# Kernel tuning notes

Measured on AMD Instinct MI355X. Metric: run time of the kernel, lower is better.

The kernel has to match this reference:

```python
import jax, jax.numpy as jnp
import numpy as np

K_MASK = -2.3819763e+38
B, T, D = 2, 2048, 2048
N, K, H = 8, 2, 256          # query heads, kv heads, head dim
F = 8192                     # ffn hidden
A = 4                        # num_altup_inputs
P = 4                        # num_modalities
WINDOW = 512
SOFT_CAP = 50.0
Q_SCALE = H ** -0.5
ROPE_BASE = 10000.0


def rms_norm(x, scale=None, eps=1e-6):
    y = x * jax.lax.rsqrt(jnp.mean(jnp.square(x), axis=-1, keepdims=True) + eps)
    if scale is not None:
        y = y * (1.0 + scale)   # scale_plus_one=True
    return y


def apply_rope(x, pos, base=ROPE_BASE, scale_factor=1.0):
    # x: [B,T,num_heads,H], pos: [B,T]
    h = x.shape[-1]
    frac = 2.0 * jnp.arange(h // 2, dtype=jnp.float32) / h
    timescale = base ** frac
    sin_inp = (pos[..., None].astype(jnp.float32) / timescale)[..., None, :] / scale_factor  # [B,T,1,H/2]
    sin, cos = jnp.sin(sin_inp), jnp.cos(sin_inp)
    x1, x2 = jnp.split(x, 2, axis=-1)
    return jnp.concatenate([x1 * cos - x2 * sin, x2 * cos + x1 * sin], axis=-1).astype(x.dtype)


def setup_inputs():
    key = jax.random.key(0)
    ks = jax.random.split(key, 12)
    r = lambda i, shape, s=0.02: jax.random.normal(ks[i], shape, dtype=jnp.float32) * s
    pos = jnp.broadcast_to(jnp.arange(T, dtype=jnp.int32), (B, T))
    causal = pos[:, :, None] >= pos[:, None, :]  # [B,T,T] bool
    return dict(
        x=jax.random.normal(ks[0], (A, B, T, D), dtype=jnp.float32),
        segment_pos=pos,
        attn_mask=causal,
        router_w=r(1, (D, P), 1.0),
        pred_coefs=r(2, (P, A, A), 0.0001),
        corr_coefs=r(3, (P, A), 0.01),
        correct_output_scale=jnp.ones((D,), jnp.float32),
        pre_attn_scale=jnp.zeros((D,), jnp.float32),
        q_w=r(4, (N, D, H)),
        kv_w=r(5, (2, K, D, H)),
        qk_q_scale=jnp.zeros((H,), jnp.float32),
        qk_k_scale=jnp.zeros((H,), jnp.float32),
        o_w=r(6, (N, H, D)),
        post_attn_scale=jnp.zeros((D,), jnp.float32),
        pre_ffw_scale=jnp.zeros((D,), jnp.float32),
        gate_w=r(7, (D, F)),
        up_w=r(8, (D, F)),
        down_w=r(9, (F, D)),
        post_ffw_scale=jnp.zeros((D,), jnp.float32),
    )


def _router(h, router_w):
    # modality router: scale by 1/d_model, project, tanh in fp32
    return jnp.tanh(jnp.einsum('btd,dp->btp', h * (1.0 / D), router_w).astype(jnp.float32))


def _attention(x, segment_pos, attn_mask, q_w, kv_w, qk_q_scale, qk_k_scale, o_w):
    q = jnp.einsum('btd,ndh->btnh', x, q_w)               # [B,T,N,H]
    k, v = jnp.einsum('bsd,ckdh->cbskh', x, kv_w)         # each [B,T,K,H]
    q = rms_norm(q, qk_q_scale)                           # qk norm
    k = rms_norm(k, qk_k_scale)
    v = rms_norm(v)                                       # value norm (no scale)
    q = apply_rope(q, segment_pos) * Q_SCALE
    k = apply_rope(k, segment_pos)
    g = N // K                                            # GQA group size
    qr = q.reshape(B, T, K, g, H)
    logits = jnp.einsum('btkgh,bskh->btkgs', qr, k).reshape(B, T, N, T)
    logits = jnp.tanh(logits / SOFT_CAP) * SOFT_CAP       # attn_logits_soft_cap
    # sliding-window mask combined with causal attn_mask
    sliding = (segment_pos[:, None, :] > segment_pos[:, :, None] - WINDOW) & \
              (segment_pos[:, None, :] < segment_pos[:, :, None] + WINDOW)
    mask = attn_mask & sliding
    padded = jnp.where(mask[:, :, None, :], logits, K_MASK)
    probs = jax.nn.softmax(padded, axis=-1).astype(k.dtype)
    enc = jnp.einsum('btkgs,bskh->btkgh', probs.reshape(B, T, K, g, T), v).reshape(B, T, N, H)
    return jnp.einsum('btnh,nhd->btd', enc, o_w)


def reference(x, segment_pos, attn_mask, router_w, pred_coefs, corr_coefs,
              correct_output_scale, pre_attn_scale, q_w, kv_w, qk_q_scale, qk_k_scale,
              o_w, post_attn_scale, pre_ffw_scale, gate_w, up_w, down_w, post_ffw_scale):
    # ---- AltUp predict ----
    mods = _router(x[0], router_w)                                   # [B,T,P]
    coefs = jnp.einsum('btp,pij->btij', mods, pred_coefs.astype(jnp.float32))
    predictions = x + jnp.einsum('btij,jbtd->ibtd', coefs, x).astype(x.dtype)
    active = predictions[0]
    # ---- attention block ----
    attn_in = rms_norm(active, pre_attn_scale)
    attn = _attention(attn_in, segment_pos, attn_mask, q_w, kv_w, qk_q_scale, qk_k_scale, o_w)
    attn = rms_norm(attn, post_attn_scale)
    attn_gated = active + attn
    # ---- gated-GELU MLP ----
    h = rms_norm(attn_gated, pre_ffw_scale)
    ffw = jnp.einsum('btf,fd->btd', jax.nn.gelu(h @ gate_w) * (h @ up_w), down_w)
    ffw = rms_norm(ffw, post_ffw_scale)
    activated = attn_gated + ffw
    # ---- AltUp correct (with scale_corrected_output) ----
    activated = activated * correct_output_scale
    mods_c = _router(activated, router_w)
    c = jnp.einsum('btp,pi->bti', mods_c, corr_coefs.astype(jnp.float32)) + 1.0
    innovation = activated - predictions[0]
    corrected = predictions + jnp.einsum('bti,btd->ibtd', c, innovation).astype(x.dtype)
    return corrected
```

## Files before the change

### kernel.cpp

```cpp
#include <hip/hip_runtime.h>
#include <hip/hip_bf16.h>

typedef unsigned short u16;
typedef __attribute__((ext_vector_type(8))) short bf16x8_t;
typedef __attribute__((ext_vector_type(4))) float f32x4_t;

#define DEV __device__ __forceinline__

constexpr int cB = 2, cT = 2048, cD = 2048;
constexpr int cN = 8, cK = 2, cH = 256, cF = 8192;
constexpr int cBT = cB * cT;
constexpr float cEPS = 1e-6f;
constexpr float cQS = 0.0625f;
constexpr float cCAP = 50.0f;
constexpr int cWIN = 512;
constexpr int cNH = 12;

DEV u16 f2bf(float f) {
  union { float f; unsigned u; } c; c.f = f;
  unsigned u = c.u;
  return (u16)((u + 0x7fffu + ((u >> 16) & 1u)) >> 16);
}
DEV float bf2f(u16 h) {
  union { unsigned u; float f; } c; c.u = ((unsigned)h) << 16;
  return c.f;
}
DEV float g4(const float4& v, int k) { return k == 0 ? v.x : k == 1 ? v.y : k == 2 ? v.z : v.w; }
DEV void store_bf4(u16* p, float a, float b, float c, float d) {
  union { u16 h[4]; uint2 v; } o;
  o.h[0] = f2bf(a); o.h[1] = f2bf(b); o.h[2] = f2bf(c); o.h[3] = f2bf(d);
  *(uint2*)p = o.v;
}
DEV float gelu_tanh(float x) {
  return 0.5f * x * (1.0f + tanhf(0.7978845608f * (x + 0.044715f * x * x * x)));
}

DEV float block_sum256(float v, float* sbuf) {
  #pragma unroll
  for (int m = 32; m > 0; m >>= 1) v += __shfl_xor(v, m, 64);
  int wid = threadIdx.x >> 6;
  if ((threadIdx.x & 63) == 0) sbuf[wid] = v;
  __syncthreads();
  float tot = sbuf[0] + sbuf[1] + sbuf[2] + sbuf[3];
  __syncthreads();
  return tot;
}

#define GLD_LDS16(gp, lp) __builtin_amdgcn_global_load_lds( \
    (const __attribute__((address_space(1))) void*)(gp),    \
    (__attribute__((address_space(3))) void*)(lp), 16, 0, 0)

#define WAITV(n) asm volatile("s_waitcnt vmcnt(" #n ")" ::: "memory")

__global__ __launch_bounds__(256) void k_transpose_cast(
    const float* __restrict__ src, u16* __restrict__ dst, int R, int C, int gu) {
  __shared__ float tile[32][33];
  size_t base = (size_t)blockIdx.z * R * C;
  int c0 = blockIdx.x * 32, r0 = blockIdx.y * 32;
  int tx = threadIdx.x & 31, ty = threadIdx.x >> 5;
  #pragma unroll
  for (int i = 0; i < 4; i++)
    tile[ty + i * 8][tx] = src[base + (size_t)(r0 + ty + i * 8) * C + c0 + tx];
  __syncthreads();
  #pragma unroll
  for (int i = 0; i < 4; i++) {
    int c = c0 + ty + i * 8;
    int n = (gu < 0) ? c : (((c >> 4) << 5) + (gu << 4) + (c & 15));
    dst[base + (size_t)n * R + r0 + tx] = f2bf(tile[tx][ty + i * 8]);
  }
}

__global__ __launch_bounds__(256) void k_predict(
    const float* __restrict__ x, const float* __restrict__ router_w,
    const float* __restrict__ pred_coefs, const float* __restrict__ pre_attn_scale,
    float* __restrict__ out, u16* __restrict__ attn_in) {
  __shared__ float sbuf[4];
  int bt = blockIdx.x, tid = threadIdx.x;
  const size_t PL = (size_t)cBT * cD;
  const size_t rowb = (size_t)bt * cD;
  float4 xv[4][2];
  #pragma unroll
  for (int j = 0; j < 4; j++)
    #pragma unroll
    for (int u = 0; u < 2; u++)
      xv[j][u] = *(const float4*)(x + j * PL + rowb + (u * 256 + tid) * 4);
  float rp[4] = {0, 0, 0, 0};
  #pragma unroll
  for (int u = 0; u < 2; u++)
    #pragma unroll
    for (int k = 0; k < 4; k++) {
      int e = (u * 256 + tid) * 4 + k;
      float4 rw = *(const float4*)(router_w + (size_t)e * 4);
      float xe = g4(xv[0][u], k);
      rp[0] += xe * rw.x; rp[1] += xe * rw.y; rp[2] += xe * rw.z; rp[3] += xe * rw.w;
    }
  float mods[4];
  #pragma unroll
  for (int p = 0; p < 4; p++) mods[p] = tanhf(block_sum256(rp[p], sbuf) * (1.0f / cD));
  float coef[4][4];
  #pragma unroll
  for (int i = 0; i < 4; i++)
    #pragma unroll
    for (int j = 0; j < 4; j++) {
      float s = 0;
      #pragma unroll
      for (int p = 0; p < 4; p++) s += mods[p] * pred_coefs[(p * 4 + i) * 4 + j];
      coef[i][j] = s;
    }
  float4 p04[2]; float ssq = 0;
  #pragma unroll
  for (int u = 0; u < 2; u++)
    #pragma unroll
    for (int i = 0; i < 4; i++) {
      float4 s = xv[i][u];
      #pragma unroll
      for (int j = 0; j < 4; j++) {
        s.x += coef[i][j] * xv[j][u].x; s.y += coef[i][j] * xv[j][u].y;
        s.z += coef[i][j] * xv[j][u].z; s.w += coef[i][j] * xv[j][u].w;
      }
      *(float4*)(out + i * PL + rowb + (u * 256 + tid) * 4) = s;
      if (i == 0) { p04[u] = s; ssq += s.x * s.x + s.y * s.y + s.z * s.z + s.w * s.w; }
    }
  float rs = rsqrtf(block_sum256(ssq, sbuf) * (1.0f / cD) + cEPS);
  #pragma unroll
  for (int u = 0; u < 2; u++) {
    int e0 = (u * 256 + tid) * 4;
    float4 sc = *(const float4*)(pre_attn_scale + e0);
    store_bf4(attn_in + rowb + e0,
              p04[u].x * rs * (1.0f + sc.x), p04[u].y * rs * (1.0f + sc.y),
              p04[u].z * rs * (1.0f + sc.z), p04[u].w * rs * (1.0f + sc.w));
  }
}

template <int MI, int OUT_MODE>
__global__ __launch_bounds__(512, 2) void k_gemm8(
    const u16* __restrict__ A, const u16* __restrict__ Bt, void* __restrict__ Cv,
    int Nn, int Kk) {
  static_assert(MI == 4 || MI == 8, "");
  constexpr int BM = MI * 32;
  constexpr int A_KS = BM * 32;
  constexpr int B_KS = 256 * 32;
  constexpr int BUF_E = 2 * A_KS + 2 * B_KS;
  extern __shared__ u16 lds[];

  const int tid = threadIdx.x;
  const int wid = tid >> 6, lane = tid & 63;
  const int wr = wid >> 2, wc = wid & 3;
  const int fr = lane & 15, fq = lane >> 4;

  const int nwg = gridDim.x * gridDim.y;
  const int flat = blockIdx.y * gridDim.x + blockIdx.x;
  const int swz = (flat & 7) * (nwg >> 3) + (flat >> 3);
  const int m0 = (swz % gridDim.x) * BM;
  const int n0 = (swz / gridDim.x) * 256;
  const int NT = Kk >> 6;

  const int srow = lane >> 2, sslot = lane & 3;

  auto stageA = [&](int t, int ks) {
    u16* buf = lds + (t & 1) * BUF_E + ks * A_KS;
    #pragma unroll
    for (int i = 0; i < BM / 128; i++) {
      int row0 = i * 128 + wid * 16;
      int row = row0 + srow;
      int col = (sslot ^ ((row >> 1) & 3)) * 8;
      GLD_LDS16(A + (size_t)(m0 + row) * Kk + t * 64 + ks * 32 + col, buf + row0 * 32);
    }
  };
  auto stageB = [&](int t, int ks) {
    u16* buf = lds + (t & 1) * BUF_E + 2 * A_KS + ks * B_KS;
    #pragma unroll
    for (int i = 0; i < 2; i++) {
      int row0 = i * 128 + wid * 16;
      int row = row0 + srow;
      int col = (sslot ^ ((row >> 1) & 3)) * 8;
      GLD_LDS16(Bt + (size_t)(n0 + row) * Kk + t * 64 + ks * 32 + col, buf + row0 * 32);
    }
  };
  auto readA = [&](const u16* buf, int ks, int i) -> bf16x8_t {
    int row = wr * (MI * 16) + i * 16 + fr;
    return *(const bf16x8_t*)(buf + ks * A_KS + row * 32 + (fq ^ ((row >> 1) & 3)) * 8);
  };
  auto readB = [&](const u16* buf, int ks, int j) -> bf16x8_t {
    int row = wc * 64 + j * 16 + fr;
    return *(const bf16x8_t*)(buf + 2 * A_KS + ks * B_KS + row * 32 + (fq ^ ((row >> 1) & 3)) * 8);
  };

  f32x4_t acc[MI][4];
  #pragma unroll
  for (int i = 0; i < MI; i++)
    #pragma unroll
    for (int j = 0; j < 4; j++) acc[i][j] = (f32x4_t){0.f, 0.f, 0.f, 0.f};

  stageA(0, 0); stageB(0, 0); stageA(0, 1); stageB(0, 1);
  if constexpr (MI == 8) WAITV(4); else WAITV(3);
  __builtin_amdgcn_s_barrier();

#define PHASE_MFMA(J0)                                                              \
  __builtin_amdgcn_s_setprio(1);                                                    \
  _Pragma("unroll")                                                                 \
  for (int i = 0; i < MI; i++) {                                                    \
    acc[i][J0]     = __builtin_amdgcn_mfma_f32_16x16x32_bf16(a0[i], b0[0], acc[i][J0], 0, 0, 0);     \
    acc[i][J0 + 1] = __builtin_amdgcn_mfma_f32_16x16x32_bf16(a0[i], b0[1], acc[i][J0 + 1], 0, 0, 0); \
  }                                                                                 \
  __builtin_amdgcn_s_setprio(0);

  for (int t = 0; t < NT; t++) {
    const u16* buf = lds + (t & 1) * BUF_E;
    const bool pf = (t + 1 < NT);
    bf16x8_t a0[MI], b0[2];

    #pragma unroll
    for (int i = 0; i < MI; i++) a0[i] = readA(buf, 0, i);
    b0[0] = readB(buf, 0, 0); b0[1] = readB(buf, 0, 1);
    if (pf) stageA(t + 1, 0);
    __builtin_amdgcn_s_barrier();
    PHASE_MFMA(0)
    __builtin_amdgcn_s_barrier();

    b0[0] = readB(buf, 0, 2); b0[1] = readB(buf, 0, 3);
    if (pf) stageB(t + 1, 0);
    if (pf) { if constexpr (MI == 8) WAITV(4); else WAITV(3); } else WAITV(0);
    __builtin_amdgcn_s_barrier();
    PHASE_MFMA(2)
    __builtin_amdgcn_s_barrier();

    #pragma unroll
    for (int i = 0; i < MI; i++) a0[i] = readA(buf, 1, i);
    b0[0] = readB(buf, 1, 0); b0[1] = readB(buf, 1, 1);
    if (pf) stageA(t + 1, 1);
    __builtin_amdgcn_s_barrier();
    PHASE_MFMA(0)
    __builtin_amdgcn_s_barrier();

    b0[0] = readB(buf, 1, 2); b0[1] = readB(buf, 1, 3);
    if (pf) stageB(t + 1, 1);
    if (pf) { if constexpr (MI == 8) WAITV(4); else WAITV(3); }
    __builtin_amdgcn_s_barrier();
    PHASE_MFMA(2)
    __builtin_amdgcn_s_barrier();
  }
#undef PHASE_MFMA

  if constexpr (OUT_MODE == 2) {
    const int Nh = Nn >> 1;
    #pragma unroll
    for (int i = 0; i < MI; i++)
      #pragma unroll
      for (int jp = 0; jp < 2; jp++) {
        int c = (n0 + wc * 64 + jp * 32) / 2 + fr;
        #pragma unroll
        for (int r = 0; r < 4; r++) {
          int m = m0 + wr * (MI * 16) + i * 16 + fq * 4 + r;
          float g = acc[i][2 * jp][r], uu = acc[i][2 * jp + 1][r];
          ((u16*)Cv)[(size_t)m * Nh + c] = f2bf(gelu_tanh(g) * uu);
        }
      }
  } else {
    #pragma unroll
    for (int i = 0; i < MI; i++)
      #pragma unroll
      for (int j = 0; j < 4; j++)
        #pragma unroll
        for (int r = 0; r < 4; r++) {
          int m = m0 + wr * (MI * 16) + i * 16 + fq * 4 + r;
          int n = n0 + wc * 64 + j * 16 + fr;
          float v = acc[i][j][r];
          if (OUT_MODE == 1) ((u16*)Cv)[(size_t)m * Nn + n] = f2bf(v);
          else ((float*)Cv)[(size_t)m * Nn + n] = v;
        }
  }
}

__global__ __launch_bounds__(64) void k_qkpost(
    u16* __restrict__ buf, const float* __restrict__ scale, const int* __restrict__ pos,
    int heads, int tokstride, int headoff, float oscale) {
  int hidx = blockIdx.x % heads, bt = blockIdx.x / heads;
  int lane = threadIdx.x;
  u16* row = buf + ((size_t)bt * tokstride + headoff + hidx) * cH;
  float v[4], ssq = 0;
  #pragma unroll
  for (int m = 0; m < 4; m++) { v[m] = bf2f(row[lane + 64 * m]); ssq += v[m] * v[m]; }
  #pragma unroll
  for (int mm = 32; mm > 0; mm >>= 1) ssq += __shfl_xor(ssq, mm, 64);
  float rs = rsqrtf(ssq * (1.0f / cH) + cEPS);
  #pragma unroll
  for (int m = 0; m < 4; m++) {
    int e = lane + 64 * m;
    v[m] = v[m] * rs * (1.0f + scale[e]);
  }
  float p = (float)pos[bt];
  #pragma unroll
  for (int m = 0; m < 2; m++) {
    int j = lane + 64 * m;
    float ts = powf(10000.0f, (2.0f * j) * (1.0f / cH));
    float si = p / ts;
    float sn = sinf(si), cs = cosf(si);
    float x1 = v[m], x2 = v[m + 2];
    row[j]       = f2bf((x1 * cs - x2 * sn) * oscale);
    row[j + 128] = f2bf((x2 * cs + x1 * sn) * oscale);
  }
}

__global__ __launch_bounds__(64) void k_vpost(
    const u16* __restrict__ qkv, u16* __restrict__ vT) {
  int kk = blockIdx.x % cK, bt = blockIdx.x / cK;
  int b = bt / cT, t = bt % cT;
  int lane = threadIdx.x;
  const u16* row = qkv + ((size_t)bt * cNH + 10 + kk) * cH;
  float v[4], ssq = 0;
  #pragma unroll
  for (int m = 0; m < 4; m++) { v[m] = bf2f(row[lane + 64 * m]); ssq += v[m] * v[m]; }
  #pragma unroll
  for (int mm = 32; mm > 0; mm >>= 1) ssq += __shfl_xor(ssq, mm, 64);
  float rs = rsqrtf(ssq * (1.0f / cH) + cEPS);
  #pragma unroll
  for (int m = 0; m < 4; m++) {
    int e = lane + 64 * m;
    vT[((size_t)(b * cK + kk) * cH + e) * cT + t] = f2bf(v[m] * rs);
  }
}

__global__ __launch_bounds__(64) void k_attn(
    const u16* __restrict__ qkv, const u16* __restrict__ vT, u16* __restrict__ enc) {
  int t0 = blockIdx.x * 16;
  int n = blockIdx.y, b = blockIdx.z;
  int kn = n >> 2;
  int lane = threadIdx.x;
  int fr = lane & 15, fq = lane >> 4;
  __shared__ float P[16][32];

  bf16x8_t qf[8];
  const u16* qrow = qkv + ((size_t)(b * cT + t0 + fr) * cNH + n) * cH;
  #pragma unroll
  for (int ks = 0; ks < 8; ks++) qf[ks] = *(const bf16x8_t*)(qrow + ks * 32 + fq * 8);

  f32x4_t acc[16];
  #pragma unroll
  for (int ht = 0; ht < 16; ht++) acc[ht] = (f32x4_t){0.f, 0.f, 0.f, 0.f};
  float psum[4] = {0.f, 0.f, 0.f, 0.f};

  int s_lo = t0 - (cWIN - 1); if (s_lo < 0) s_lo = 0; s_lo &= ~31;
  for (int s0 = s_lo; s0 <= t0 + 15; s0 += 32) {
    f32x4_t S[2];
    S[0] = (f32x4_t){0.f, 0.f, 0.f, 0.f};
    S[1] = (f32x4_t){0.f, 0.f, 0.f, 0.f};
    #pragma unroll
    for (int c = 0; c < 2; c++) {
      const u16* krow = qkv + ((size_t)(b * cT + s0 + c * 16 + fr) * cNH + 8 + kn) * cH;
      #pragma unroll
      for (int ks = 0; ks < 8; ks++) {
        bf16x8_t kf = *(const bf16x8_t*)(krow + ks * 32 + fq * 8);
        S[c] = __builtin_amdgcn_mfma_f32_16x16x32_bf16(qf[ks], kf, S[c], 0, 0, 0);
      }
    }
    #pragma unroll
    for (int c = 0; c < 2; c++) {
      int s = s0 + c * 16 + fr;
      #pragma unroll
      for (int r = 0; r < 4; r++) {
        int t = t0 + fq * 4 + r;
        float l = S[c][r];
        l = tanhf(l * (1.0f / cCAP)) * cCAP;
        float pe = (s <= t && s >= t - (cWIN - 1)) ? __expf(l) : 0.0f;
        psum[r] += pe;
        P[fq * 4 + r][c * 16 + fr] = pe;
      }
    }
    bf16x8_t pf;
    #pragma unroll
    for (int e = 0; e < 8; e++) pf[e] = (short)f2bf(P[fr][fq * 8 + e]);
    #pragma unroll
    for (int ht = 0; ht < 16; ht++) {
      bf16x8_t vf = *(const bf16x8_t*)(vT + (((size_t)(b * cK + kn)) * cH + ht * 16 + fr) * cT + s0 + fq * 8);
      acc[ht] = __builtin_amdgcn_mfma_f32_16x16x32_bf16(pf, vf, acc[ht], 0, 0, 0);
    }
  }
  #pragma unroll
  for (int r = 0; r < 4; r++) {
    #pragma unroll
    for (int m = 1; m < 16; m <<= 1) psum[r] += __shfl_xor(psum[r], m, 64);
  }
  float inv[4];
  #pragma unroll
  for (int r = 0; r < 4; r++) inv[r] = 1.0f / psum[r];
  #pragma unroll
  for (int ht = 0; ht < 16; ht++)
    #pragma unroll
    for (int r = 0; r < 4; r++)
      enc[(((size_t)(b * cT + t0 + fq * 4 + r)) * cN + n) * cH + ht * 16 + fr] =
          f2bf(acc[ht][r] * inv[r]);
}

__global__ __launch_bounds__(256) void k_postattn(
    const float* __restrict__ attn_raw, const float* __restrict__ out0,
    const float* __restrict__ post_attn_scale, const float* __restrict__ pre_ffw_scale,
    float* __restrict__ ag, u16* __restrict__ h) {
  __shared__ float sbuf[4];
  int bt = blockIdx.x, tid = threadIdx.x;
  const size_t rowb = (size_t)bt * cD;
  float4 ar[2]; float ssq = 0;
  #pragma unroll
  for (int u = 0; u < 2; u++) {
    ar[u] = *(const float4*)(attn_raw + rowb + (u * 256 + tid) * 4);
    ssq += ar[u].x * ar[u].x + ar[u].y * ar[u].y + ar[u].z * ar[u].z + ar[u].w * ar[u].w;
  }
  float rs = rsqrtf(block_sum256(ssq, sbuf) * (1.0f / cD) + cEPS);
  float4 agv[2]; float ssq2 = 0;
  #pragma unroll
  for (int u = 0; u < 2; u++) {
    int e0 = (u * 256 + tid) * 4;
    float4 o0 = *(const float4*)(out0 + rowb + e0);
    float4 sc = *(const float4*)(post_attn_scale + e0);
    float4 a;
    a.x = o0.x + ar[u].x * rs * (1.0f + sc.x);
    a.y = o0.y + ar[u].y * rs * (1.0f + sc.y);
    a.z = o0.z + ar[u].z * rs * (1.0f + sc.z);
    a.w = o0.w + ar[u].w * rs * (1.0f + sc.w);
    agv[u] = a;
    *(float4*)(ag + rowb + e0) = a;
    ssq2 += a.x * a.x + a.y * a.y + a.z * a.z + a.w * a.w;
  }
  float rs2 = rsqrtf(block_sum256(ssq2, sbuf) * (1.0f / cD) + cEPS);
  #pragma unroll
  for (int u = 0; u < 2; u++) {
    int e0 = (u * 256 + tid) * 4;
    float4 sc = *(const float4*)(pre_ffw_scale + e0);
    store_bf4(h + rowb + e0,
              agv[u].x * rs2 * (1.0f + sc.x), agv[u].y * rs2 * (1.0f + sc.y),
              agv[u].z * rs2 * (1.0f + sc.z), agv[u].w * rs2 * (1.0f + sc.w));
  }
}

__global__ __launch_bounds__(256) void k_final(
    const float* __restrict__ ffw_raw, const float* __restrict__ ag,
    const float* __restrict__ post_ffw_scale, const float* __restrict__ cos_scale,
    const float* __restrict__ router_w, const float* __restrict__ corr_coefs,
    float* __restrict__ out) {
  __shared__ float sbuf[4];
  int bt = blockIdx.x, tid = threadIdx.x;
  const size_t PL = (size_t)cBT * cD;
  const size_t rowb = (size_t)bt * cD;
  float4 fv[2]; float ssq = 0;
  #pragma unroll
  for (int u = 0; u < 2; u++) {
    fv[u] = *(const float4*)(ffw_raw + rowb + (u * 256 + tid) * 4);
    ssq += fv[u].x * fv[u].x + fv[u].y * fv[u].y + fv[u].z * fv[u].z + fv[u].w * fv[u].w;
  }
  float rs = rsqrtf(block_sum256(ssq, sbuf) * (1.0f / cD) + cEPS);
  float4 av[2];
  float rp[4] = {0, 0, 0, 0};
  #pragma unroll
  for (int u = 0; u < 2; u++) {
    int e0 = (u * 256 + tid) * 4;
    float4 agx = *(const float4*)(ag + rowb + e0);
    float4 ps = *(const float4*)(post_ffw_scale + e0);
    float4 cs = *(const float4*)(cos_scale + e0);
    float4 a;
    a.x = (agx.x + fv[u].x * rs * (1.0f + ps.x)) * cs.x;
    a.y = (agx.y + fv[u].y * rs * (1.0f + ps.y)) * cs.y;
    a.z = (agx.z + fv[u].z * rs * (1.0f + ps.z)) * cs.z;
    a.w = (agx.w + fv[u].w * rs * (1.0f + ps.w)) * cs.w;
    av[u] = a;
    #pragma unroll
    for (int k = 0; k < 4; k++) {
      float4 rw = *(const float4*)(router_w + (size_t)(e0 + k) * 4);
      float xe = g4(a, k);
      rp[0] += xe * rw.x; rp[1] += xe * rw.y; rp[2] += xe * rw.z; rp[3] += xe * rw.w;
    }
  }
  float mods[4];
  #pragma unroll
  for (int p = 0; p < 4; p++) mods[p] = tanhf(block_sum256(rp[p], sbuf) * (1.0f / cD));
  float cc[4];
  #pragma unroll
  for (int i = 0; i < 4; i++) {
    float s = 1.0f;
    #pragma unroll
    for (int p = 0; p < 4; p++) s += mods[p] * corr_coefs[p * 4 + i];
    cc[i] = s;
  }
  #pragma unroll
  for (int u = 0; u < 2; u++) {
    size_t o = rowb + (u * 256 + tid) * 4;
    float4 p0 = *(const float4*)(out + o);
    float4 in4;
    in4.x = av[u].x - p0.x; in4.y = av[u].y - p0.y;
    in4.z = av[u].z - p0.z; in4.w = av[u].w - p0.w;
    float4 w0;
    w0.x = p0.x + cc[0] * in4.x; w0.y = p0.y + cc[0] * in4.y;
    w0.z = p0.z + cc[0] * in4.z; w0.w = p0.w + cc[0] * in4.w;
    *(float4*)(out + o) = w0;
    #pragma unroll
    for (int i = 1; i < 4; i++) {
      float4 q = *(const float4*)(out + i * PL + o);
      q.x += cc[i] * in4.x; q.y += cc[i] * in4.y;
      q.z += cc[i] * in4.z; q.w += cc[i] * in4.w;
      *(float4*)(out + i * PL + o) = q;
    }
  }
}

extern "C" void kernel_launch(void* const* d_in, const int* in_sizes, int n_in,
                              void* d_out, int out_size, void* d_ws, size_t ws_size,
                              hipStream_t stream) {
  const float* x              = (const float*)d_in[0];
  const int*   pos            = (const int*)d_in[1];
  const float* router_w       = (const float*)d_in[3];
  const float* pred_coefs     = (const float*)d_in[4];
  const float* corr_coefs     = (const float*)d_in[5];
  const float* cos_scale      = (const float*)d_in[6];
  const float* pre_attn_scale = (const float*)d_in[7];
  const float* q_w            = (const float*)d_in[8];
  const float* kv_w           = (const float*)d_in[9];
  const float* qk_q_scale     = (const float*)d_in[10];
  const float* qk_k_scale     = (const float*)d_in[11];
  const float* o_w            = (const float*)d_in[12];
  const float* post_attn_scale= (const float*)d_in[13];
  const float* pre_ffw_scale  = (const float*)d_in[14];
  const float* gate_w         = (const float*)d_in[15];
  const float* up_w           = (const float*)d_in[16];
  const float* down_w         = (const float*)d_in[17];
  const float* post_ffw_scale = (const float*)d_in[18];
  float* out = (float*)d_out;

  char* wsp = (char*)d_ws;
  size_t off = 0;
  auto take = [&](size_t nbytes) -> char* {
    char* p = wsp + off;
    off += (nbytes + 255) & ~((size_t)255);
    return p;
  };
  u16* gu_wT    = (u16*)take((size_t)2 * cF * cD * 2);
  u16* down_wT  = (u16*)take((size_t)cD * cF * 2);
  u16* qkv_wT   = (u16*)take((size_t)cNH * cH * cD * 2);
  u16* o_wT     = (u16*)take((size_t)cD * cN * cH * 2);
  u16* attn_in  = (u16*)take((size_t)cBT * cD * 2);
  u16* qkvbuf   = (u16*)take((size_t)cBT * cNH * cH * 2);
  u16* vTbuf    = (u16*)take((size_t)cB * cK * cH * cT * 2);
  u16* encbuf   = (u16*)take((size_t)cBT * cN * cH * 2);
  float* attn_raw = (float*)take((size_t)cBT * cD * 4);
  float* agbuf    = (float*)take((size_t)cBT * cD * 4);
  u16* hbuf     = (u16*)take((size_t)cBT * cD * 2);
  u16* Gcbuf    = (u16*)take((size_t)cBT * cF * 2);
  float* ffw_raw = (float*)take((size_t)cBT * cD * 4);
  (void)in_sizes; (void)n_in; (void)out_size; (void)ws_size;

  dim3 blk256(256), blk64(64), blk512(512);
  constexpr unsigned LDS8 = 2 * (2 * 256 * 32 + 2 * 256 * 32) * 2;
  constexpr unsigned LDS4 = 2 * (2 * 128 * 32 + 2 * 256 * 32) * 2;

  k_transpose_cast<<<dim3(cF / 32, cD / 32, 1), blk256, 0, stream>>>(gate_w, gu_wT, cD, cF, 0);
  k_transpose_cast<<<dim3(cF / 32, cD / 32, 1), blk256, 0, stream>>>(up_w, gu_wT, cD, cF, 1);
  k_transpose_cast<<<dim3(cD / 32, cF / 32, 1), blk256, 0, stream>>>(down_w, down_wT, cF, cD, -1);
  k_transpose_cast<<<dim3(cH / 32, cD / 32, cN), blk256, 0, stream>>>(q_w, qkv_wT, cD, cH, -1);
  k_transpose_cast<<<dim3(cH / 32, cD / 32, 2 * cK), blk256, 0, stream>>>(
      kv_w, qkv_wT + (size_t)cN * cH * cD, cD, cH, -1);
  k_transpose_cast<<<dim3(cD / 32, (cN * cH) / 32, 1), blk256, 0, stream>>>(o_w, o_wT, cN * cH, cD, -1);

  k_predict<<<dim3(cBT), blk256, 0, stream>>>(x, router_w, pred_coefs, pre_attn_scale, out, attn_in);

  k_gemm8<4, 1><<<dim3(cBT / 128, (cNH * cH) / 256), blk512, LDS4, stream>>>(
      attn_in, qkv_wT, qkvbuf, cNH * cH, cD);

  k_qkpost<<<dim3(cBT * cN), blk64, 0, stream>>>(qkvbuf, qk_q_scale, pos, cN, cNH, 0, cQS);
  k_qkpost<<<dim3(cBT * cK), blk64, 0, stream>>>(qkvbuf, qk_k_scale, pos, cK, cNH, 8, 1.0f);
  k_vpost<<<dim3(cBT * cK), blk64, 0, stream>>>(qkvbuf, vTbuf);

  k_attn<<<dim3(cT / 16, cN, cB), blk64, 0, stream>>>(qkvbuf, vTbuf, encbuf);

  k_gemm8<4, 0><<<dim3(cBT / 128, cD / 256), blk512, LDS4, stream>>>(
      encbuf, o_wT, attn_raw, cD, cN * cH);
  k_postattn<<<dim3(cBT), blk256, 0, stream>>>(attn_raw, out, post_attn_scale, pre_ffw_scale, agbuf, hbuf);

  k_gemm8<8, 2><<<dim3(cBT / 256, (2 * cF) / 256), blk512, LDS8, stream>>>(
      hbuf, gu_wT, Gcbuf, 2 * cF, cD);
  k_gemm8<4, 0><<<dim3(cBT / 128, cD / 256), blk512, LDS4, stream>>>(
      Gcbuf, down_wT, ffw_raw, cD, cF);

  k_final<<<dim3(cBT), blk256, 0, stream>>>(ffw_raw, agbuf, post_ffw_scale, cos_scale,
                                            router_w, corr_coefs, out);
}
```

Before: 1.005 ms.

## Precompute RoPE table, fuse q/k/v post kernels, fast tanh, reschedule GEMM prefetch

Several independent changes land together. A RoPE sin/cos table is precomputed once, and the three q/k/v post-processing kernels merge into one launch that reads it. tanh and GELU switch to exp plus reciprocal approximations in the router, attention softcap and GEMM epilogue. The four block reductions become one batched reduction, and the attention P tile is padded. The GEMM main loop now issues both A and B stages for the next tile in the first two phases with adjusted vmcnt waits, which trades earlier prefetch for more loads in flight and some accuracy loss from the approximations.

```diff
diff --git a/kernel.cpp b/kernel.cpp
--- a/kernel.cpp
+++ b/kernel.cpp
@@ -31,8 +31,14 @@
   o.h[0] = f2bf(a); o.h[1] = f2bf(b); o.h[2] = f2bf(c); o.h[3] = f2bf(d);
   *(uint2*)p = o.v;
 }
-DEV float gelu_tanh(float x) {
-  return 0.5f * x * (1.0f + tanhf(0.7978845608f * (x + 0.044715f * x * x * x)));
+DEV float tanh_fast(float x) {
+  float e2 = __expf(2.0f * x);
+  return 1.0f - 2.0f * __builtin_amdgcn_rcpf(e2 + 1.0f);
+}
+DEV float gelu_fast(float x) {
+  float u = 1.5957691216057308f * (x + 0.044715f * x * x * x);
+  float e2 = __expf(u);
+  return x * (1.0f - __builtin_amdgcn_rcpf(e2 + 1.0f));
 }
 
 DEV float block_sum256(float v, float* sbuf) {
@@ -45,6 +51,19 @@
   __syncthreads();
   return tot;
 }
+DEV void block_sum256x4(float v[4], float* sbuf ) {
+  #pragma unroll
+  for (int m = 32; m > 0; m >>= 1) {
+    #pragma unroll
+    for (int k = 0; k < 4; k++) v[k] += __shfl_xor(v[k], m, 64);
+  }
+  int wid = threadIdx.x >> 6;
+  if ((threadIdx.x & 63) == 0) *(float4*)(sbuf + wid * 4) = make_float4(v[0], v[1], v[2], v[3]);
+  __syncthreads();
+  #pragma unroll
+  for (int k = 0; k < 4; k++) v[k] = sbuf[k] + sbuf[4 + k] + sbuf[8 + k] + sbuf[12 + k];
+  __syncthreads();
+}
 
 #define GLD_LDS16(gp, lp) __builtin_amdgcn_global_load_lds( \
     (const __attribute__((address_space(1))) void*)(gp),    \
@@ -70,11 +89,21 @@
   }
 }
 
+__global__ __launch_bounds__(256) void k_rope_table(
+    const int* __restrict__ pos, float2* __restrict__ rt) {
+  int idx = blockIdx.x * 256 + threadIdx.x;
+  int bt = idx >> 7, j = idx & 127;
+  float p = (float)pos[bt];
+  float ts = powf(10000.0f, (2.0f * j) * (1.0f / cH));
+  float si = p / ts;
+  rt[idx] = make_float2(sinf(si), cosf(si));
+}
+
 __global__ __launch_bounds__(256) void k_predict(
     const float* __restrict__ x, const float* __restrict__ router_w,
     const float* __restrict__ pred_coefs, const float* __restrict__ pre_attn_scale,
     float* __restrict__ out, u16* __restrict__ attn_in) {
-  __shared__ float sbuf[4];
+  __shared__ float sbuf[16];
   int bt = blockIdx.x, tid = threadIdx.x;
   const size_t PL = (size_t)cBT * cD;
   const size_t rowb = (size_t)bt * cD;
@@ -94,9 +123,10 @@
       float xe = g4(xv[0][u], k);
       rp[0] += xe * rw.x; rp[1] += xe * rw.y; rp[2] += xe * rw.z; rp[3] += xe * rw.w;
     }
+  block_sum256x4(rp, sbuf);
   float mods[4];
   #pragma unroll
-  for (int p = 0; p < 4; p++) mods[p] = tanhf(block_sum256(rp[p], sbuf) * (1.0f / cD));
+  for (int p = 0; p < 4; p++) mods[p] = tanh_fast(rp[p] * (1.0f / cD));
   float coef[4][4];
   #pragma unroll
   for (int i = 0; i < 4; i++)
@@ -213,14 +243,15 @@
     #pragma unroll
     for (int i = 0; i < MI; i++) a0[i] = readA(buf, 0, i);
     b0[0] = readB(buf, 0, 0); b0[1] = readB(buf, 0, 1);
-    if (pf) stageA(t + 1, 0);
+    if (pf) { stageA(t + 1, 0); stageB(t + 1, 0); }
+    asm volatile("" ::: "memory");
     __builtin_amdgcn_s_barrier();
     PHASE_MFMA(0)
     __builtin_amdgcn_s_barrier();
 
     b0[0] = readB(buf, 0, 2); b0[1] = readB(buf, 0, 3);
-    if (pf) stageB(t + 1, 0);
-    if (pf) { if constexpr (MI == 8) WAITV(4); else WAITV(3); } else WAITV(0);
+    if (pf) { stageA(t + 1, 1); stageB(t + 1, 1); }
+    if (pf) { if constexpr (MI == 8) WAITV(8); else WAITV(6); } else WAITV(0);
     __builtin_amdgcn_s_barrier();
     PHASE_MFMA(2)
     __builtin_amdgcn_s_barrier();
@@ -228,13 +259,11 @@
     #pragma unroll
     for (int i = 0; i < MI; i++) a0[i] = readA(buf, 1, i);
     b0[0] = readB(buf, 1, 0); b0[1] = readB(buf, 1, 1);
-    if (pf) stageA(t + 1, 1);
     __builtin_amdgcn_s_barrier();
     PHASE_MFMA(0)
     __builtin_amdgcn_s_barrier();
 
     b0[0] = readB(buf, 1, 2); b0[1] = readB(buf, 1, 3);
-    if (pf) stageB(t + 1, 1);
     if (pf) { if constexpr (MI == 8) WAITV(4); else WAITV(3); }
     __builtin_amdgcn_s_barrier();
     PHASE_MFMA(2)
@@ -253,7 +282,7 @@
         for (int r = 0; r < 4; r++) {
           int m = m0 + wr * (MI * 16) + i * 16 + fq * 4 + r;
           float g = acc[i][2 * jp][r], uu = acc[i][2 * jp + 1][r];
-          ((u16*)Cv)[(size_t)m * Nh + c] = f2bf(gelu_tanh(g) * uu);
+          ((u16*)Cv)[(size_t)m * Nh + c] = f2bf(gelu_fast(g) * uu);
         }
       }
   } else {
@@ -272,52 +301,43 @@
   }
 }
 
-__global__ __launch_bounds__(64) void k_qkpost(
-    u16* __restrict__ buf, const float* __restrict__ scale, const int* __restrict__ pos,
-    int heads, int tokstride, int headoff, float oscale) {
-  int hidx = blockIdx.x % heads, bt = blockIdx.x / heads;
+__global__ __launch_bounds__(64) void k_qkvpost(
+    u16* __restrict__ qkv, const float* __restrict__ qscale,
+    const float* __restrict__ kscale, const float2* __restrict__ rt,
+    u16* __restrict__ vT) {
+  int h = blockIdx.x % cNH, bt = blockIdx.x / cNH;
   int lane = threadIdx.x;
-  u16* row = buf + ((size_t)bt * tokstride + headoff + hidx) * cH;
+  u16* row = qkv + ((size_t)bt * cNH + h) * cH;
   float v[4], ssq = 0;
   #pragma unroll
   for (int m = 0; m < 4; m++) { v[m] = bf2f(row[lane + 64 * m]); ssq += v[m] * v[m]; }
   #pragma unroll
   for (int mm = 32; mm > 0; mm >>= 1) ssq += __shfl_xor(ssq, mm, 64);
   float rs = rsqrtf(ssq * (1.0f / cH) + cEPS);
-  #pragma unroll
-  for (int m = 0; m < 4; m++) {
-    int e = lane + 64 * m;
-    v[m] = v[m] * rs * (1.0f + scale[e]);
-  }
-  float p = (float)pos[bt];
-  #pragma unroll
-  for (int m = 0; m < 2; m++) {
-    int j = lane + 64 * m;
-    float ts = powf(10000.0f, (2.0f * j) * (1.0f / cH));
-    float si = p / ts;
-    float sn = sinf(si), cs = cosf(si);
-    float x1 = v[m], x2 = v[m + 2];
-    row[j]       = f2bf((x1 * cs - x2 * sn) * oscale);
-    row[j + 128] = f2bf((x2 * cs + x1 * sn) * oscale);
-  }
-}
-
-__global__ __launch_bounds__(64) void k_vpost(
-    const u16* __restrict__ qkv, u16* __restrict__ vT) {
-  int kk = blockIdx.x % cK, bt = blockIdx.x / cK;
-  int b = bt / cT, t = bt % cT;
-  int lane = threadIdx.x;
-  const u16* row = qkv + ((size_t)bt * cNH + 10 + kk) * cH;
-  float v[4], ssq = 0;
-  #pragma unroll
-  for (int m = 0; m < 4; m++) { v[m] = bf2f(row[lane + 64 * m]); ssq += v[m] * v[m]; }
-  #pragma unroll
-  for (int mm = 32; mm > 0; mm >>= 1) ssq += __shfl_xor(ssq, mm, 64);
-  float rs = rsqrtf(ssq * (1.0f / cH) + cEPS);
-  #pragma unroll
-  for (int m = 0; m < 4; m++) {
-    int e = lane + 64 * m;
-    vT[((size_t)(b * cK + kk) * cH + e) * cT + t] = f2bf(v[m] * rs);
+  if (h < 10) {
+    const float* sc = (h < 8) ? qscale : kscale;
+    float os = (h < 8) ? cQS : 1.0f;
+    #pragma unroll
+    for (int m = 0; m < 4; m++) {
+      int e = lane + 64 * m;
+      v[m] = v[m] * rs * (1.0f + sc[e]);
+    }
+    #pragma unroll
+    for (int m = 0; m < 2; m++) {
+      int j = lane + 64 * m;
+      float2 t = rt[bt * 128 + j];
+      float x1 = v[m], x2 = v[m + 2];
+      row[j]       = f2bf((x1 * t.y - x2 * t.x) * os);
+      row[j + 128] = f2bf((x2 * t.y + x1 * t.x) * os);
+    }
+  } else {
+    int kk = h - 10;
+    int b = bt / cT, t = bt % cT;
+    #pragma unroll
+    for (int m = 0; m < 4; m++) {
+      int e = lane + 64 * m;
+      vT[((size_t)(b * cK + kk) * cH + e) * cT + t] = f2bf(v[m] * rs);
+    }
   }
 }
 
@@ -328,7 +348,7 @@
   int kn = n >> 2;
   int lane = threadIdx.x;
   int fr = lane & 15, fq = lane >> 4;
-  __shared__ float P[16][32];
+  __shared__ float P[16][33];
 
   bf16x8_t qf[8];
   const u16* qrow = qkv + ((size_t)(b * cT + t0 + fr) * cNH + n) * cH;
@@ -360,8 +380,7 @@
       #pragma unroll
       for (int r = 0; r < 4; r++) {
         int t = t0 + fq * 4 + r;
-        float l = S[c][r];
-        l = tanhf(l * (1.0f / cCAP)) * cCAP;
+        float l = cCAP * tanh_fast(S[c][r] * (1.0f / cCAP));
         float pe = (s <= t && s >= t - (cWIN - 1)) ? __expf(l) : 0.0f;
         psum[r] += pe;
         P[fq * 4 + r][c * 16 + fr] = pe;
@@ -437,7 +456,7 @@
     const float* __restrict__ post_ffw_scale, const float* __restrict__ cos_scale,
     const float* __restrict__ router_w, const float* __restrict__ corr_coefs,
     float* __restrict__ out) {
-  __shared__ float sbuf[4];
+  __shared__ float sbuf[16];
   int bt = blockIdx.x, tid = threadIdx.x;
   const size_t PL = (size_t)cBT * cD;
   const size_t rowb = (size_t)bt * cD;
@@ -469,15 +488,13 @@
       rp[0] += xe * rw.x; rp[1] += xe * rw.y; rp[2] += xe * rw.z; rp[3] += xe * rw.w;
     }
   }
-  float mods[4];
-  #pragma unroll
-  for (int p = 0; p < 4; p++) mods[p] = tanhf(block_sum256(rp[p], sbuf) * (1.0f / cD));
+  block_sum256x4(rp, sbuf);
   float cc[4];
   #pragma unroll
   for (int i = 0; i < 4; i++) {
     float s = 1.0f;
     #pragma unroll
-    for (int p = 0; p < 4; p++) s += mods[p] * corr_coefs[p * 4 + i];
+    for (int p = 0; p < 4; p++) s += tanh_fast(rp[p] * (1.0f / cD)) * corr_coefs[p * 4 + i];
     cc[i] = s;
   }
   #pragma unroll
@@ -544,6 +561,7 @@
   u16* hbuf     = (u16*)take((size_t)cBT * cD * 2);
   u16* Gcbuf    = (u16*)take((size_t)cBT * cF * 2);
   float* ffw_raw = (float*)take((size_t)cBT * cD * 4);
+  float2* ropetab = (float2*)take((size_t)cBT * 128 * 8);
   (void)in_sizes; (void)n_in; (void)out_size; (void)ws_size;
 
   dim3 blk256(256), blk64(64), blk512(512);
@@ -557,15 +575,14 @@
   k_transpose_cast<<<dim3(cH / 32, cD / 32, 2 * cK), blk256, 0, stream>>>(
       kv_w, qkv_wT + (size_t)cN * cH * cD, cD, cH, -1);
   k_transpose_cast<<<dim3(cD / 32, (cN * cH) / 32, 1), blk256, 0, stream>>>(o_w, o_wT, cN * cH, cD, -1);
+  k_rope_table<<<dim3(cBT * 128 / 256), blk256, 0, stream>>>(pos, ropetab);
 
   k_predict<<<dim3(cBT), blk256, 0, stream>>>(x, router_w, pred_coefs, pre_attn_scale, out, attn_in);
 
   k_gemm8<4, 1><<<dim3(cBT / 128, (cNH * cH) / 256), blk512, LDS4, stream>>>(
       attn_in, qkv_wT, qkvbuf, cNH * cH, cD);
 
-  k_qkpost<<<dim3(cBT * cN), blk64, 0, stream>>>(qkvbuf, qk_q_scale, pos, cN, cNH, 0, cQS);
-  k_qkpost<<<dim3(cBT * cK), blk64, 0, stream>>>(qkvbuf, qk_k_scale, pos, cK, cNH, 8, 1.0f);
-  k_vpost<<<dim3(cBT * cK), blk64, 0, stream>>>(qkvbuf, vTbuf);
+  k_qkvpost<<<dim3(cBT * cNH), blk64, 0, stream>>>(qkvbuf, qk_q_scale, qk_k_scale, ropetab, vTbuf);
 
   k_attn<<<dim3(cT / 16, cN, cB), blk64, 0, stream>>>(qkvbuf, vTbuf, encbuf);
 
```

Measured after the change: 1.040 ms. 3.5% more time.
